# Kernel optimization log

Measured on AMD Instinct MI355X. Metric: run time of the kernel, lower is better.

## Reference

```python
import jax, jax.numpy as jnp
import numpy as np
import math

PAD = 0
EPS = 1e-5


def _mha(x, ids, num_heads, qw, qb, kw, kb, vw, vb, pw, pb):
    # Faithful vectorization of the per-head Python loop: identical math per head.
    B, S, D = x.shape
    d = D // num_heads
    q = (x @ qw + qb).reshape(B, S, num_heads, d)
    k = (x @ kw + kb).reshape(B, S, num_heads, d)
    v = (x @ vw + vb).reshape(B, S, num_heads, d)
    scores = jnp.einsum('bqhd,bkhd->bhqk', q, k) / math.sqrt(d)
    key_mask = (ids != PAD)[:, None, None, :]  # mask padded KEYS only (as in source)
    scores = jnp.where(key_mask, scores, -jnp.inf)
    w = jax.nn.softmax(scores, axis=-1)
    out = jnp.einsum('bhqk,bkhd->bqhd', w, v).reshape(B, S, D)
    return out @ pw + pb + x  # projection + residual


def setup_inputs() -> dict:
    V, D, B, S = 50257, 1024, 64, 512
    key = jax.random.key(0)
    ks = jax.random.split(key, 24)
    s = 0.02

    def lin(k, din, dout):
        k1, k2 = jax.random.split(k)
        return (jax.random.normal(k1, (din, dout), jnp.float32) * s,
                jax.random.normal(k2, (dout,), jnp.float32) * s)

    x = jax.random.randint(ks[0], (B, S), 0, V, dtype=jnp.int64)
    emb_w = jax.random.normal(ks[1], (V, D), jnp.float32) * s
    pos_w = jax.random.normal(ks[2], (512, D), jnp.float32) * s
    a1_qw, a1_qb = lin(ks[3], D, D)
    a1_kw, a1_kb = lin(ks[4], D, D)
    a1_vw, a1_vb = lin(ks[5], D, D)
    a1_pw, a1_pb = lin(ks[6], D, D)
    a2_qw, a2_qb = lin(ks[7], D, D)
    a2_kw, a2_kb = lin(ks[8], D, D)
    a2_vw, a2_vb = lin(ks[9], D, D)
    a2_pw, a2_pb = lin(ks[10], D, D)
    norm_g = jnp.ones((D,), jnp.float32)
    norm_b = jnp.zeros((D,), jnp.float32)
    lin_w, lin_b = lin(ks[11], D, 1)
    return dict(x=x, emb_w=emb_w, pos_w=pos_w,
                a1_qw=a1_qw, a1_qb=a1_qb, a1_kw=a1_kw, a1_kb=a1_kb,
                a1_vw=a1_vw, a1_vb=a1_vb, a1_pw=a1_pw, a1_pb=a1_pb,
                a2_qw=a2_qw, a2_qb=a2_qb, a2_kw=a2_kw, a2_kb=a2_kb,
                a2_vw=a2_vw, a2_vb=a2_vb, a2_pw=a2_pw, a2_pb=a2_pb,
                norm_g=norm_g, norm_b=norm_b, lin_w=lin_w, lin_b=lin_b)


def reference(x, emb_w, pos_w,
              a1_qw, a1_qb, a1_kw, a1_kb, a1_vw, a1_vb, a1_pw, a1_pb,
              a2_qw, a2_qb, a2_kw, a2_kb, a2_vw, a2_vb, a2_pw, a2_pb,
              norm_g, norm_b, lin_w, lin_b):
    B, S = x.shape
    h = emb_w[x] + pos_w[jnp.arange(S)][None, :, :]  # word + positional emb
    res_emb = h
    h = _mha(h, x, 8, a1_qw, a1_qb, a1_kw, a1_kb, a1_vw, a1_vb, a1_pw, a1_pb)
    # dropout is identity in eval
    h = _mha(h, x, 4, a2_qw, a2_qb, a2_kw, a2_kb, a2_vw, a2_vb, a2_pw, a2_pb)
    h = h + res_emb
    # mean pooling over non-pad tokens (type=0 branch)
    m = (x != PAD)[:, :, None].astype(h.dtype)
    pooled = jnp.sum(h * m, axis=1) / jnp.sum(m, axis=1)
    # LayerNorm
    mu = jnp.mean(pooled, axis=-1, keepdims=True)
    var = jnp.mean((pooled - mu) ** 2, axis=-1, keepdims=True)
    normed = (pooled - mu) / jnp.sqrt(var + EPS) * norm_g + norm_b
    return normed @ lin_w + lin_b  # [B, 1]
```

## Files before the change

### kernel.cpp

```cpp
#include <hip/hip_runtime.h>

typedef unsigned short u16;
typedef short short8 __attribute__((ext_vector_type(8)));
typedef unsigned short u16x8 __attribute__((ext_vector_type(8)));
typedef float f32x4 __attribute__((ext_vector_type(4)));
typedef const __attribute__((address_space(1))) void* gptr_t;
typedef __attribute__((address_space(3))) void* lptr_t;

#define B_  64
#define S_  512
#define D_  1024
#define BS_ (B_*S_)

__device__ __forceinline__ float b2f(u16 v) {
    union { float f; unsigned u; } c; c.u = ((unsigned)v) << 16; return c.f;
}
__device__ __forceinline__ u16 f2b(float f) {
    union { float f; unsigned u; } c; c.f = f;
    unsigned r = c.u + 0x7FFFu + ((c.u >> 16) & 1u);
    return (u16)(r >> 16);
}

__global__ void detect_k(const u16* __restrict__ raw, int* __restrict__ flag) {
    __shared__ int cnt;
    if (threadIdx.x == 0) cnt = 0;
    __syncthreads();
    u16 v = raw[threadIdx.x * 2];
    int e = (v >> 7) & 0xFF;
    int sane = (e >= 64 && e <= 150) ? 1 : 0;
    atomicAdd(&cnt, sane);
    __syncthreads();
    if (threadIdx.x == 0) *flag = (cnt >= 192) ? 1 : 0;
}

__global__ __launch_bounds__(256) void convert_params_k(
    const void* b0, const void* b1, const void* b2, const void* b3,
    const void* b4, const void* b5, const void* b6, const void* b7,
    const void* g, const void* be, const void* lw, const void* lb,
    const int* __restrict__ flagp, u16* __restrict__ dst)
{
    const void* srcs[12] = {b0, b1, b2, b3, b4, b5, b6, b7, g, be, lw, lb};
    int slot = blockIdx.x;
    int n = (slot == 11) ? 1 : 1024;
    int f = *flagp;
    const void* s = srcs[slot];
    for (int i = threadIdx.x; i < n; i += 256) {
        float v = f ? b2f(((const u16*)s)[i]) : ((const float*)s)[i];
        dst[slot * 1024 + i] = f2b(v);
    }
}

__global__ __launch_bounds__(256) void transpose_k(const void* __restrict__ W,
                                                   u16* __restrict__ Wt,
                                                   const int* __restrict__ flagp) {
    __shared__ float t[32][33];
    int f = *flagp;
    int tx = threadIdx.x, ty = threadIdx.y;
    int x0 = blockIdx.x * 32, y0 = blockIdx.y * 32;
    for (int i = ty; i < 32; i += 8) {
        size_t idx = (size_t)(y0 + i) * D_ + x0 + tx;
        t[i][tx] = f ? b2f(((const u16*)W)[idx]) : ((const float*)W)[idx];
    }
    __syncthreads();
    for (int i = ty; i < 32; i += 8)
        Wt[(size_t)(x0 + i) * D_ + y0 + tx] = f2b(t[tx][i]);
}

__global__ __launch_bounds__(256) void embed_k(const int* __restrict__ x, const void* __restrict__ emb,
                                               const void* __restrict__ pos, u16* __restrict__ h0,
                                               const int* __restrict__ flagp) {
    int f = *flagp;
    int bs = blockIdx.x;
    int s = bs & (S_ - 1);
    int tok = x[bs];
    u16* orow = h0 + (size_t)bs * D_;
    int c = threadIdx.x * 4;
    float e0, e1, e2, e3, p0, p1, p2, p3;
    if (f) {
        ushort4 e = *(const ushort4*)((const u16*)emb + (size_t)tok * D_ + c);
        ushort4 p = *(const ushort4*)((const u16*)pos + (size_t)s * D_ + c);
        e0 = b2f(e.x); e1 = b2f(e.y); e2 = b2f(e.z); e3 = b2f(e.w);
        p0 = b2f(p.x); p1 = b2f(p.y); p2 = b2f(p.z); p3 = b2f(p.w);
    } else {
        float4 e = *(const float4*)((const float*)emb + (size_t)tok * D_ + c);
        float4 p = *(const float4*)((const float*)pos + (size_t)s * D_ + c);
        e0 = e.x; e1 = e.y; e2 = e.z; e3 = e.w;
        p0 = p.x; p1 = p.y; p2 = p.z; p3 = p.w;
    }
    ushort4 o;
    o.x = f2b(e0 + p0); o.y = f2b(e1 + p1); o.z = f2b(e2 + p2); o.w = f2b(e3 + p3);
    *(ushort4*)(orow + c) = o;
}

template <int NT>
__global__ __launch_bounds__(512, 2) void gemm256_k(
    const u16* __restrict__ A, const u16* __restrict__ Bt,
    const u16* __restrict__ bias,
    const u16* __restrict__ res, const u16* __restrict__ res2,
    u16* __restrict__ Cq, u16* __restrict__ Ck, u16* __restrict__ Vt)
{
    int bid = blockIdx.x;
    int xcd = bid & 7;
    int loc = bid >> 3;
    int chunk = loc >> 6;
    int r = loc & 63;
    int mt = xcd * 16 + (r >> 2);
    int nt = chunk * 4 + (r & 3);
    int m0 = mt * 256, n0 = nt * 256;

    int tid = threadIdx.x;
    int lane = tid & 63, wid = tid >> 6, quad = lane >> 4, l16 = lane & 15;
    int wm = wid >> 2, wn = wid & 3;
    int pxor = l16 & 7;

    __shared__ __align__(16) u16 lds[2][2][2][128 * 64];

    f32x4 acc[8][4];
#pragma unroll
    for (int i = 0; i < 8; i++)
#pragma unroll
        for (int j = 0; j < 4; j++) acc[i][j] = (f32x4){0.f, 0.f, 0.f, 0.f};

    int srow = tid >> 3;
    int skof = ((tid & 7) ^ (srow & 7)) * 8;

    auto STAGE_HALF = [&](int kt, int mat, int hlf) {
        int p = kt & 1;
        int kbase = kt * 64;
        const u16* src = (mat == 0)
            ? A  + (size_t)(m0 + hlf * 128) * D_ + kbase
            : Bt + (size_t)(n0 + hlf * 128) * D_ + kbase;
        u16* dst = &lds[p][mat][hlf][0];
        __builtin_amdgcn_global_load_lds((gptr_t)(src + (size_t)srow * D_ + skof),
                                         (lptr_t)(dst + tid * 8), 16, 0, 0);
        __builtin_amdgcn_global_load_lds((gptr_t)(src + (size_t)(srow + 64) * D_ + skof),
                                         (lptr_t)(dst + 4096 + tid * 8), 16, 0, 0);
    };

    STAGE_HALF(0, 0, 0); STAGE_HALF(0, 0, 1);
    STAGE_HALF(0, 1, 0); STAGE_HALF(0, 1, 1);
    STAGE_HALF(1, 1, 0); STAGE_HALF(1, 1, 1);
    asm volatile("s_waitcnt vmcnt(4)" ::: "memory");
    __builtin_amdgcn_s_barrier();

    int brow0 = (wn & 1) * 64;
    for (int kt = 0; kt < 16; ++kt) {
        int p = kt & 1;
        const u16* Ah = &lds[p][0][wm][0];
        const u16* Bh = &lds[p][1][wn >> 1][0];
        short8 bf[4][2];
#pragma unroll
        for (int q = 0; q < 4; ++q) {
            if (q == 0) {
#pragma unroll
                for (int nj = 0; nj < 4; ++nj)
#pragma unroll
                    for (int kh = 0; kh < 2; ++kh)
                        bf[nj][kh] = *(const short8*)&Bh[(brow0 + nj * 16 + l16) * 64 +
                                                         ((kh * 4 + quad) ^ pxor) * 8];
            }
            short8 af[2][2];
#pragma unroll
            for (int mi2 = 0; mi2 < 2; ++mi2)
#pragma unroll
                for (int kh = 0; kh < 2; ++kh)
                    af[mi2][kh] = *(const short8*)&Ah[((2 * q + mi2) * 16 + l16) * 64 +
                                                      ((kh * 4 + quad) ^ pxor) * 8];
            if (q == 0 && kt + 1 < 16) STAGE_HALF(kt + 1, 0, 0);
            if (q == 1 && kt + 1 < 16) STAGE_HALF(kt + 1, 0, 1);
            if (q == 2 && kt + 2 < 16) STAGE_HALF(kt + 2, 1, 0);
            if (q == 3 && kt + 2 < 16) STAGE_HALF(kt + 2, 1, 1);
            __builtin_amdgcn_s_barrier();
            asm volatile("s_waitcnt lgkmcnt(0)" ::: "memory");
            __builtin_amdgcn_sched_barrier(0);
            __builtin_amdgcn_s_setprio(1);
#pragma unroll
            for (int kh = 0; kh < 2; ++kh)
#pragma unroll
                for (int mi2 = 0; mi2 < 2; ++mi2)
#pragma unroll
                    for (int nj = 0; nj < 4; ++nj)
                        acc[2 * q + mi2][nj] = __builtin_amdgcn_mfma_f32_16x16x32_bf16(
                            af[mi2][kh], bf[nj][kh], acc[2 * q + mi2][nj], 0, 0, 0);
            __builtin_amdgcn_s_setprio(0);
            __builtin_amdgcn_s_barrier();
        }
        if (kt < 15) {
            if (kt < 14) asm volatile("s_waitcnt vmcnt(4)" ::: "memory");
            else         asm volatile("s_waitcnt vmcnt(0)" ::: "memory");
            __builtin_amdgcn_s_barrier();
        }
    }

    __syncthreads();
    float* fl = (float*)(&lds[0][0][0][0]) + wid * 1104;

    int nbase = n0 + wn * 64;
    bool vwave = (NT == 12) && (nbase >= 2048);

    if (vwave) {
        int colv = nbase + lane - 2048;
        float bv = b2f(bias[nbase + lane]);
#pragma unroll
        for (int mi = 0; mi < 8; ++mi) {
#pragma unroll
            for (int nj = 0; nj < 4; ++nj)
                *(f32x4*)&fl[(nj * 16 + l16) * 17 + quad * 4] = acc[mi][nj];
            asm volatile("s_waitcnt lgkmcnt(0)" ::: "memory");
            int rowbase = m0 + wm * 128 + mi * 16;
            int bb = rowbase >> 9, sb0 = rowbase & (S_ - 1);
            u16x8 o0, o1;
#pragma unroll
            for (int s = 0; s < 8; ++s) {
                o0[s] = f2b(fl[lane * 17 + s] + bv);
                o1[s] = f2b(fl[lane * 17 + 8 + s] + bv);
            }
            u16* dst = Vt + ((size_t)bb * D_ + colv) * S_ + sb0;
            *(u16x8*)dst = o0;
            *(u16x8*)(dst + 8) = o1;
            asm volatile("" ::: "memory");
        }
    } else {
        u16* Cd = (NT == 12 && nbase >= 1024) ? Ck : Cq;
        int rr2 = lane >> 2, sg = lane & 3;
        float bvv[2][8];
#pragma unroll
        for (int g = 0; g < 2; ++g) {
            u16x8 b8 = *(const u16x8*)&bias[nbase + sg * 8 + g * 32];
#pragma unroll
            for (int j = 0; j < 8; ++j) bvv[g][j] = b2f(b8[j]);
        }
#pragma unroll
        for (int mi = 0; mi < 8; ++mi) {
#pragma unroll
            for (int nj = 0; nj < 4; ++nj)
                *(f32x4*)&fl[(nj * 16 + l16) * 17 + quad * 4] = acc[mi][nj];
            asm volatile("s_waitcnt lgkmcnt(0)" ::: "memory");
            int row_g = m0 + wm * 128 + mi * 16 + rr2;
#pragma unroll
            for (int g = 0; g < 2; ++g) {
                int c0 = sg * 8 + g * 32;
                int colc = (nbase + c0) & 1023;
                size_t idx = (size_t)row_g * D_ + colc;
                float v[8];
#pragma unroll
                for (int j = 0; j < 8; ++j)
                    v[j] = fl[(c0 + j) * 17 + rr2] + bvv[g][j];
                if (res) {
                    u16x8 r8 = *(const u16x8*)&res[idx];
#pragma unroll
                    for (int j = 0; j < 8; ++j) v[j] += b2f(r8[j]);
                }
                if (res2) {
                    u16x8 r8 = *(const u16x8*)&res2[idx];
#pragma unroll
                    for (int j = 0; j < 8; ++j) v[j] += b2f(r8[j]);
                }
                u16x8 o;
#pragma unroll
                for (int j = 0; j < 8; ++j) o[j] = f2b(v[j]);
                *(u16x8*)&Cd[idx] = o;
            }
            asm volatile("" ::: "memory");
        }
    }
}

template <int HD, int NBUF>
__global__ __launch_bounds__(512, HD == 128 ? 4 : 2) void attn8_k(
    const u16* Q, const u16* __restrict__ Kn, const u16* __restrict__ Vt,
    const int* __restrict__ x, u16* O, int H)
{
    constexpr int NKF = HD / 32, NOF = HD / 16;
    constexpr int KP = HD + 8;
    constexpr int VP = (HD == 256 && NBUF == 2) ? 36 : 40;
    constexpr int KC = (32 * HD / 8) / 512;
    constexpr int VC = (HD * 32 / 8) / 512;
    const float scale = (HD == 128) ? 0.08838834764831845f : 0.0625f;
    int bh = blockIdx.x;
    int b = bh / H, h = bh - b * H;
    int tid = threadIdx.x, wid = tid >> 6, lane = tid & 63, quad = lane >> 4, l16 = lane & 15;
    int qrow = blockIdx.y * 128 + wid * 16;

    const u16* Qb = Q + (size_t)(b * S_) * D_ + h * HD;
    const u16* Kb = Kn + (size_t)(b * S_) * D_ + h * HD;
    const u16* Vb = Vt + ((size_t)b * D_ + h * HD) * S_;
    const int* xb = x + b * S_;

    __shared__ __align__(16) u16 Ks[NBUF][32 * KP];
    __shared__ __align__(16) u16 Vs[NBUF][HD * VP];
    __shared__ __align__(16) u16 Pl[8 * 16 * 32];

    short8 qf[NKF];
#pragma unroll
    for (int f = 0; f < NKF; ++f)
        qf[f] = *(const short8*)(Qb + (size_t)(qrow + l16) * D_ + f * 32 + quad * 8);

    f32x4 of[NOF];
    float lpart[4];
#pragma unroll
    for (int f = 0; f < NOF; ++f) of[f] = (f32x4){0.f, 0.f, 0.f, 0.f};
#pragma unroll
    for (int r = 0; r < 4; ++r) lpart[r] = 0.f;

    short8 kreg[KC], vreg[VC];
    auto LOADKV = [&](int key0) {
#pragma unroll
        for (int i = 0; i < KC; ++i) {
            int c = tid + i * 512;
            int row = c / (HD / 8), col = (c % (HD / 8)) * 8;
            kreg[i] = *(const short8*)(Kb + (size_t)(key0 + row) * D_ + col);
        }
#pragma unroll
        for (int i = 0; i < VC; ++i) {
            int c = tid + i * 512;
            int row = c >> 2, col = (c & 3) * 8;
            vreg[i] = *(const short8*)(Vb + (size_t)row * S_ + key0 + col);
        }
    };

    LOADKV(0);

    for (int t = 0; t < 16; ++t) {
        int key0 = t * 32;
        int p = (NBUF == 2) ? (t & 1) : 0;
        if (NBUF == 1) __syncthreads();
#pragma unroll
        for (int i = 0; i < KC; ++i) {
            int c = tid + i * 512;
            int row = c / (HD / 8), col = (c % (HD / 8)) * 8;
            *(short8*)&Ks[p][row * KP + col] = kreg[i];
        }
#pragma unroll
        for (int i = 0; i < VC; ++i) {
            int c = tid + i * 512;
            int row = c >> 2, col = (c & 3) * 8;
            *(short8*)&Vs[p][row * VP + col] = vreg[i];
        }
        if (key0 + 32 < S_) LOADKV(key0 + 32);
        int tok0 = xb[key0 + l16] != 0;
        int tok1 = xb[key0 + 16 + l16] != 0;
        __syncthreads();

        f32x4 sc0 = (f32x4){0.f, 0.f, 0.f, 0.f};
        f32x4 sc1 = (f32x4){0.f, 0.f, 0.f, 0.f};
#pragma unroll
        for (int f = 0; f < NKF; ++f) {
            short8 k0 = *(const short8*)&Ks[p][l16 * KP + f * 32 + quad * 8];
            short8 k1 = *(const short8*)&Ks[p][(16 + l16) * KP + f * 32 + quad * 8];
            sc0 = __builtin_amdgcn_mfma_f32_16x16x32_bf16(qf[f], k0, sc0, 0, 0, 0);
            sc1 = __builtin_amdgcn_mfma_f32_16x16x32_bf16(qf[f], k1, sc1, 0, 0, 0);
        }
#pragma unroll
        for (int r = 0; r < 4; ++r) {
            float p0 = tok0 ? __expf(sc0[r] * scale) : 0.f;
            float p1 = tok1 ? __expf(sc1[r] * scale) : 0.f;
            lpart[r] += p0 + p1;
            Pl[wid * 512 + (quad * 4 + r) * 32 + l16] = f2b(p0);
            Pl[wid * 512 + (quad * 4 + r) * 32 + 16 + l16] = f2b(p1);
        }
        __asm volatile("s_waitcnt lgkmcnt(0)" ::: "memory");
        short8 pf = *(const short8*)&Pl[wid * 512 + l16 * 32 + quad * 8];
#pragma unroll
        for (int f = 0; f < NOF; ++f) {
            short8 vf = *(const short8*)&Vs[p][(f * 16 + l16) * VP + quad * 8];
            of[f] = __builtin_amdgcn_mfma_f32_16x16x32_bf16(pf, vf, of[f], 0, 0, 0);
        }
    }

    u16* Ob = O + (size_t)(b * S_) * D_ + h * HD;
    float rl[4];
#pragma unroll
    for (int r = 0; r < 4; ++r) {
        float l = lpart[r];
#pragma unroll
        for (int msk = 1; msk < 16; msk <<= 1) l += __shfl_xor(l, msk, 64);
        rl[r] = 1.0f / l;
    }
#pragma unroll
    for (int f = 0; f < NOF; ++f)
#pragma unroll
        for (int r = 0; r < 4; ++r)
            Ob[(size_t)(qrow + quad * 4 + r) * D_ + f * 16 + l16] =
                f2b(of[f][r] * rl[r]);
}

__global__ __launch_bounds__(256) void pool_zero_k(float* __restrict__ pooled, int* __restrict__ cnt) {
    int b = blockIdx.x;
    for (int i = threadIdx.x; i < 1024; i += 256) pooled[b * 1024 + i] = 0.f;
    if (threadIdx.x == 0) cnt[b] = 0;
}

__global__ __launch_bounds__(256) void pool_partial_k(
    const u16* __restrict__ Hf, const int* __restrict__ x,
    float* __restrict__ pooled, int* __restrict__ cnt)
{
    int b = blockIdx.x, seg = blockIdx.y;
    int c = threadIdx.x * 4;
    const int* xb = x + b * S_;
    float a0 = 0.f, a1 = 0.f, a2 = 0.f, a3 = 0.f;
    int local = 0;
    int s0 = seg * 64;
    for (int i = 0; i < 64; ++i) {
        int s = s0 + i;
        if (xb[s] != 0) {
            ushort4 hv = *(const ushort4*)(Hf + (size_t)(b * S_ + s) * D_ + c);
            a0 += b2f(hv.x); a1 += b2f(hv.y); a2 += b2f(hv.z); a3 += b2f(hv.w);
            local++;
        }
    }
    atomicAdd(&pooled[b * 1024 + c + 0], a0);
    atomicAdd(&pooled[b * 1024 + c + 1], a1);
    atomicAdd(&pooled[b * 1024 + c + 2], a2);
    atomicAdd(&pooled[b * 1024 + c + 3], a3);
    if (threadIdx.x == 0) atomicAdd(&cnt[b], local);
}

__global__ __launch_bounds__(256) void pool_final_k(
    const float* __restrict__ pooled, const int* __restrict__ cnt,
    const u16* __restrict__ prm, void* __restrict__ out, const int* __restrict__ flagp)
{
    __shared__ float sb[8];
    const u16* g  = prm + 8 * 1024;
    const u16* be = prm + 9 * 1024;
    const u16* lw = prm + 10 * 1024;
    const u16* lb = prm + 11 * 1024;
    int b = blockIdx.x;
    int c = threadIdx.x * 4;
    int n = cnt[b];
    float inv = 1.0f / (float)(n > 0 ? n : 1);
    float p0 = pooled[b * 1024 + c + 0] * inv;
    float p1 = pooled[b * 1024 + c + 1] * inv;
    float p2 = pooled[b * 1024 + c + 2] * inv;
    float p3 = pooled[b * 1024 + c + 3] * inv;
    float s1 = p0 + p1 + p2 + p3;
    float s2 = p0 * p0 + p1 * p1 + p2 * p2 + p3 * p3;
#pragma unroll
    for (int m = 32; m >= 1; m >>= 1) { s1 += __shfl_xor(s1, m, 64); s2 += __shfl_xor(s2, m, 64); }
    int wid = threadIdx.x >> 6, lane = threadIdx.x & 63;
    if (lane == 0) { sb[wid] = s1; sb[4 + wid] = s2; }
    __syncthreads();
    float S1 = sb[0] + sb[1] + sb[2] + sb[3];
    float S2 = sb[4] + sb[5] + sb[6] + sb[7];
    float mu = S1 * (1.0f / 1024.0f);
    float var = S2 * (1.0f / 1024.0f) - mu * mu;
    float rstd = rsqrtf(var + 1e-5f);
    float dot = ((p0 - mu) * rstd * b2f(g[c + 0]) + b2f(be[c + 0])) * b2f(lw[c + 0])
              + ((p1 - mu) * rstd * b2f(g[c + 1]) + b2f(be[c + 1])) * b2f(lw[c + 1])
              + ((p2 - mu) * rstd * b2f(g[c + 2]) + b2f(be[c + 2])) * b2f(lw[c + 2])
              + ((p3 - mu) * rstd * b2f(g[c + 3]) + b2f(be[c + 3])) * b2f(lw[c + 3]);
#pragma unroll
    for (int m = 32; m >= 1; m >>= 1) dot += __shfl_xor(dot, m, 64);
    __syncthreads();
    if (lane == 0) sb[wid] = dot;
    __syncthreads();
    if (threadIdx.x == 0) {
        float v = sb[0] + sb[1] + sb[2] + sb[3] + b2f(lb[0]);
        if (*flagp) ((u16*)out)[b] = f2b(v);
        else        ((float*)out)[b] = v;
    }
}

extern "C" void kernel_launch(void* const* d_in, const int* in_sizes, int n_in,
                              void* d_out, int out_size, void* d_ws, size_t ws_size,
                              hipStream_t stream)
{
    (void)in_sizes; (void)n_in; (void)out_size; (void)ws_size;
    const int* x = (const int*)d_in[0];

    char* ws = (char*)d_ws;
    size_t off = 0;
    auto carve = [&](size_t bytes) -> char* {
        char* p = ws + off;
        off += (bytes + 255) & ~(size_t)255;
        return p;
    };
    int* flag    = (int*)carve(256);
    u16* prm     = (u16*)carve(12 * 1024 * 2);
    float* pooled = (float*)carve(64 * 1024 * 4);
    int* cnt     = (int*)carve(64 * 4);
    const size_t WB = (size_t)D_ * D_ * 2;
    const size_t HB = (size_t)BS_ * D_ * 2;
    u16* wt[8];
    for (int i = 0; i < 8; i++) wt[i] = (u16*)carve(WB);
    u16* h0   = (u16*)carve(HB);
    u16* buf2 = (u16*)carve(HB);
    u16* buf3 = (u16*)carve(HB);
    u16* buf4 = (u16*)carve(HB);
    u16* buf5 = (u16*)carve(HB);

    detect_k<<<1, 256, 0, stream>>>((const u16*)d_in[1], flag);
    convert_params_k<<<12, 256, 0, stream>>>(
        d_in[4], d_in[6], d_in[8], d_in[10], d_in[12], d_in[14], d_in[16], d_in[18],
        d_in[19], d_in[20], d_in[21], d_in[22], flag, prm);

    dim3 tb(32, 8), tg(32, 32);
    const int widx[8] = {3, 5, 7, 9, 11, 13, 15, 17};
    for (int i = 0; i < 8; i++)
        transpose_k<<<tg, tb, 0, stream>>>(d_in[widx[i]], wt[i], flag);

    embed_k<<<BS_, 256, 0, stream>>>(x, d_in[1], d_in[2], h0, flag);

    gemm256_k<12><<<1536, 512, 0, stream>>>(h0, wt[0], prm + 0 * 1024,
                                            nullptr, nullptr, buf2, buf3, buf4);
    attn8_k<128, 2><<<dim3(B_ * 8, 4), 512, 0, stream>>>(buf2, buf3, buf4, x, buf2, 8);
    gemm256_k<4><<<512, 512, 0, stream>>>(buf2, wt[3], prm + 3 * 1024,
                                          h0, nullptr, buf5, nullptr, nullptr);
    gemm256_k<12><<<1536, 512, 0, stream>>>(buf5, wt[4], prm + 4 * 1024,
                                            nullptr, nullptr, buf2, buf3, buf4);
    attn8_k<256, 2><<<dim3(B_ * 4, 4), 512, 0, stream>>>(buf2, buf3, buf4, x, buf2, 4);
    gemm256_k<4><<<512, 512, 0, stream>>>(buf2, wt[7], prm + 7 * 1024,
                                          buf5, h0, buf3, nullptr, nullptr);

    pool_zero_k<<<B_, 256, 0, stream>>>(pooled, cnt);
    pool_partial_k<<<dim3(B_, 8), 256, 0, stream>>>(buf3, x, pooled, cnt);
    pool_final_k<<<B_, 256, 0, stream>>>(pooled, cnt, prm, d_out, flag);
}
```

Before: 1.015 ms.

## Fuse masked mean-pool accumulation into final projection GEMM epilogue

The last projection GEMM no longer writes the full hidden state. Instead it masks rows by token id, reduces column partial sums across lanes and atomically adds them into the pooled buffer. The separate pool_partial kernel is removed, and pool_final now counts non-pad tokens itself. This avoids writing and re-reading a 64 MB bf16 activation, at the cost of extra shuffles and atomics in the GEMM epilogue. Summation now uses fp32 values that were never rounded to bf16.

```diff
diff --git a/kernel.cpp b/kernel.cpp
--- a/kernel.cpp
+++ b/kernel.cpp
@@ -97,7 +97,8 @@
     const u16* __restrict__ A, const u16* __restrict__ Bt,
     const u16* __restrict__ bias,
     const u16* __restrict__ res, const u16* __restrict__ res2,
-    u16* __restrict__ Cq, u16* __restrict__ Ck, u16* __restrict__ Vt)
+    u16* __restrict__ Cq, u16* __restrict__ Ck, u16* __restrict__ Vt,
+    const int* __restrict__ xm, float* __restrict__ pool)
 {
     int bid = blockIdx.x;
     int xcd = bid & 7;
@@ -230,13 +231,23 @@
 #pragma unroll
             for (int j = 0; j < 8; ++j) bvv[g][j] = b2f(b8[j]);
         }
+        float psum[2][8];
+#pragma unroll
+        for (int g = 0; g < 2; ++g)
+#pragma unroll
+            for (int j = 0; j < 8; ++j) psum[g][j] = 0.f;
+        int rowb0 = m0 + wm * 128;
+        int b_ = rowb0 >> 9;
+        const int* xb_ = pool ? (xm + b_ * S_) : nullptr;
+
 #pragma unroll
         for (int mi = 0; mi < 8; ++mi) {
 #pragma unroll
             for (int nj = 0; nj < 4; ++nj)
                 *(f32x4*)&fl[(nj * 16 + l16) * 17 + quad * 4] = acc[mi][nj];
             asm volatile("s_waitcnt lgkmcnt(0)" ::: "memory");
-            int row_g = m0 + wm * 128 + mi * 16 + rr2;
+            int row_g = rowb0 + mi * 16 + rr2;
+            int msk = pool ? (xb_[row_g & (S_ - 1)] != 0) : 0;
 #pragma unroll
             for (int g = 0; g < 2; ++g) {
                 int c0 = sg * 8 + g * 32;
@@ -256,12 +267,37 @@
 #pragma unroll
                     for (int j = 0; j < 8; ++j) v[j] += b2f(r8[j]);
                 }
-                u16x8 o;
-#pragma unroll
-                for (int j = 0; j < 8; ++j) o[j] = f2b(v[j]);
-                *(u16x8*)&Cd[idx] = o;
+                if (pool) {
+                    if (msk)
+#pragma unroll
+                        for (int j = 0; j < 8; ++j) psum[g][j] += v[j];
+                } else {
+                    u16x8 o;
+#pragma unroll
+                    for (int j = 0; j < 8; ++j) o[j] = f2b(v[j]);
+                    *(u16x8*)&Cd[idx] = o;
+                }
             }
             asm volatile("" ::: "memory");
+        }
+        if (pool) {
+#pragma unroll
+            for (int g = 0; g < 2; ++g)
+#pragma unroll
+                for (int j = 0; j < 8; ++j) {
+#pragma unroll
+                    for (int m = 4; m <= 32; m <<= 1)
+                        psum[g][j] += __shfl_xor(psum[g][j], m, 64);
+                }
+            if (rr2 == 0) {
+#pragma unroll
+                for (int g = 0; g < 2; ++g) {
+                    int colc = (nbase + sg * 8 + g * 32) & 1023;
+#pragma unroll
+                    for (int j = 0; j < 8; ++j)
+                        atomicAdd(&pool[b_ * 1024 + colc + j], psum[g][j]);
+                }
+            }
         }
     }
 }
@@ -385,49 +421,34 @@
                 f2b(of[f][r] * rl[r]);
 }
 
-__global__ __launch_bounds__(256) void pool_zero_k(float* __restrict__ pooled, int* __restrict__ cnt) {
+__global__ __launch_bounds__(256) void pool_zero_k(float* __restrict__ pooled) {
     int b = blockIdx.x;
     for (int i = threadIdx.x; i < 1024; i += 256) pooled[b * 1024 + i] = 0.f;
-    if (threadIdx.x == 0) cnt[b] = 0;
-}
-
-__global__ __launch_bounds__(256) void pool_partial_k(
-    const u16* __restrict__ Hf, const int* __restrict__ x,
-    float* __restrict__ pooled, int* __restrict__ cnt)
-{
-    int b = blockIdx.x, seg = blockIdx.y;
-    int c = threadIdx.x * 4;
-    const int* xb = x + b * S_;
-    float a0 = 0.f, a1 = 0.f, a2 = 0.f, a3 = 0.f;
-    int local = 0;
-    int s0 = seg * 64;
-    for (int i = 0; i < 64; ++i) {
-        int s = s0 + i;
-        if (xb[s] != 0) {
-            ushort4 hv = *(const ushort4*)(Hf + (size_t)(b * S_ + s) * D_ + c);
-            a0 += b2f(hv.x); a1 += b2f(hv.y); a2 += b2f(hv.z); a3 += b2f(hv.w);
-            local++;
-        }
-    }
-    atomicAdd(&pooled[b * 1024 + c + 0], a0);
-    atomicAdd(&pooled[b * 1024 + c + 1], a1);
-    atomicAdd(&pooled[b * 1024 + c + 2], a2);
-    atomicAdd(&pooled[b * 1024 + c + 3], a3);
-    if (threadIdx.x == 0) atomicAdd(&cnt[b], local);
 }
 
 __global__ __launch_bounds__(256) void pool_final_k(
-    const float* __restrict__ pooled, const int* __restrict__ cnt,
+    const float* __restrict__ pooled, const int* __restrict__ x,
     const u16* __restrict__ prm, void* __restrict__ out, const int* __restrict__ flagp)
 {
     __shared__ float sb[8];
+    __shared__ int sbi[4];
     const u16* g  = prm + 8 * 1024;
     const u16* be = prm + 9 * 1024;
     const u16* lw = prm + 10 * 1024;
     const u16* lb = prm + 11 * 1024;
     int b = blockIdx.x;
     int c = threadIdx.x * 4;
-    int n = cnt[b];
+    int wid = threadIdx.x >> 6, lane = threadIdx.x & 63;
+
+    const int* xb = x + b * S_;
+    int localc = 0;
+    for (int i = threadIdx.x; i < S_; i += 256) localc += (xb[i] != 0);
+#pragma unroll
+    for (int m = 32; m >= 1; m >>= 1) localc += __shfl_xor(localc, m, 64);
+    if (lane == 0) sbi[wid] = localc;
+    __syncthreads();
+    int n = sbi[0] + sbi[1] + sbi[2] + sbi[3];
+
     float inv = 1.0f / (float)(n > 0 ? n : 1);
     float p0 = pooled[b * 1024 + c + 0] * inv;
     float p1 = pooled[b * 1024 + c + 1] * inv;
@@ -437,7 +458,6 @@
     float s2 = p0 * p0 + p1 * p1 + p2 * p2 + p3 * p3;
 #pragma unroll
     for (int m = 32; m >= 1; m >>= 1) { s1 += __shfl_xor(s1, m, 64); s2 += __shfl_xor(s2, m, 64); }
-    int wid = threadIdx.x >> 6, lane = threadIdx.x & 63;
     if (lane == 0) { sb[wid] = s1; sb[4 + wid] = s2; }
     __syncthreads();
     float S1 = sb[0] + sb[1] + sb[2] + sb[3];
@@ -479,6 +499,7 @@
     u16* prm     = (u16*)carve(12 * 1024 * 2);
     float* pooled = (float*)carve(64 * 1024 * 4);
     int* cnt     = (int*)carve(64 * 4);
+    (void)cnt;
     const size_t WB = (size_t)D_ * D_ * 2;
     const size_t HB = (size_t)BS_ * D_ * 2;
     u16* wt[8];
@@ -501,18 +522,22 @@
 
     embed_k<<<BS_, 256, 0, stream>>>(x, d_in[1], d_in[2], h0, flag);
 
+    pool_zero_k<<<B_, 256, 0, stream>>>(pooled);
+
     gemm256_k<12><<<1536, 512, 0, stream>>>(h0, wt[0], prm + 0 * 1024,
-                                            nullptr, nullptr, buf2, buf3, buf4);
+                                            nullptr, nullptr, buf2, buf3, buf4,
+                                            nullptr, nullptr);
     attn8_k<128, 2><<<dim3(B_ * 8, 4), 512, 0, stream>>>(buf2, buf3, buf4, x, buf2, 8);
     gemm256_k<4><<<512, 512, 0, stream>>>(buf2, wt[3], prm + 3 * 1024,
-                                          h0, nullptr, buf5, nullptr, nullptr);
+                                          h0, nullptr, buf5, nullptr, nullptr,
+                                          nullptr, nullptr);
     gemm256_k<12><<<1536, 512, 0, stream>>>(buf5, wt[4], prm + 4 * 1024,
-                                            nullptr, nullptr, buf2, buf3, buf4);
+                                            nullptr, nullptr, buf2, buf3, buf4,
+                                            nullptr, nullptr);
     attn8_k<256, 2><<<dim3(B_ * 4, 4), 512, 0, stream>>>(buf2, buf3, buf4, x, buf2, 4);
     gemm256_k<4><<<512, 512, 0, stream>>>(buf2, wt[7], prm + 7 * 1024,
-                                          buf5, h0, buf3, nullptr, nullptr);
-
-    pool_zero_k<<<B_, 256, 0, stream>>>(pooled, cnt);
-    pool_partial_k<<<dim3(B_, 8), 256, 0, stream>>>(buf3, x, pooled, cnt);
-    pool_final_k<<<B_, 256, 0, stream>>>(pooled, cnt, prm, d_out, flag);
-}
+                                          buf5, h0, nullptr, nullptr, nullptr,
+                                          x, pooled);
+
+    pool_final_k<<<B_, 256, 0, stream>>>(pooled, x, prm, d_out, flag);
+}
```

After: 993.8 us. 1.02x faster.
